# Optimization experiments

Hardware: AMD Instinct MI355X
Metric: run time of the kernel (lower is better)

The kernel has to match this reference:

```python
import jax, jax.numpy as jnp
import numpy as np

# pywt db4 decomposition lowpass filter (L=8)
DB4_DEC_LO = np.array([
    -0.010597401784997278, 0.032883011666982945, 0.030841381835986965,
    -0.18703481171888114, -0.02798376941698385, 0.6308807679295904,
    0.7148465705525415, 0.23037781330885523], dtype=np.float32)


def _dwt_1d(x, dec_lo, axis):
    """Single-level 1-D DWT along `axis`, pywt 'symmetric' mode.

    Implements pywt downsampling convolution: symmetric-extend by L-1 on each
    side, correlate with reversed decomposition filters, take every 2nd sample
    starting at offset 1. out_len = floor((n + L - 1) / 2).
    """
    L = dec_lo.shape[0]
    # QMF highpass: dec_hi[n] = (-1)^(n+1) * dec_lo[L-1-n]
    signs = jnp.where(jnp.arange(L) % 2 == 0, -1.0, 1.0).astype(x.dtype)
    dec_hi = signs * dec_lo[::-1]
    lo_rev = dec_lo[::-1]  # correlation kernel = reversed conv filter
    hi_rev = dec_hi[::-1]

    x = jnp.moveaxis(x, axis, -1)
    n = x.shape[-1]
    pad = [(0, 0)] * (x.ndim - 1) + [(L - 1, L - 1)]
    xp = jnp.pad(x, pad, mode='symmetric')  # half-sample symmetric, as pywt
    out_len = (n + L - 1) // 2

    ylo = jnp.zeros(x.shape[:-1] + (out_len,), x.dtype)
    yhi = jnp.zeros(x.shape[:-1] + (out_len,), x.dtype)
    for m in range(L):  # small fixed tap count; fused by XLA
        seg = xp[..., 1 + m: 1 + m + 2 * out_len: 2]
        ylo = ylo + lo_rev[m] * seg
        yhi = yhi + hi_rev[m] * seg
    return jnp.moveaxis(ylo, -1, axis), jnp.moveaxis(yhi, -1, axis)


def setup_inputs() -> dict:
    key = jax.random.key(0)
    x = jax.random.normal(key, (8, 512, 512, 16), dtype=jnp.float32)
    dec_lo = jnp.asarray(DB4_DEC_LO)
    return {"x": x, "dec_lo": dec_lo}


def reference(x, dec_lo):
    # Separable 2-D DWT over axes [-3, -2] (channels-last [B,H,W,C]).
    a, d = _dwt_1d(x, dec_lo, axis=-3)          # lowpass/highpass along H
    aa, ad = _dwt_1d(a, dec_lo, axis=-2)        # then along W
    da, dd = _dwt_1d(d, dec_lo, axis=-2)
    return (aa, ad, da, dd)
```

## Files before the change

kernel.cpp:

```cpp
#include <hip/hip_runtime.h>


constexpr int N  = 512;
constexpr int ON = 259;
constexpr int CH = 16;
constexpr int NB = 8;
constexpr int JB = 29;
constexpr int BANDS = 9;
constexpr int RS = 16;
constexpr int SEGS = 17;
constexpr int W  = 2 * JB + 6;
constexpr int LSTR = 20;

typedef float vfloat4 __attribute__((ext_vector_type(4)));

__device__ __forceinline__ int refl(int r) {
  r = (r < 0) ? (-r - 1) : r;
  return (r >= N) ? (2 * N - 1 - r) : r;
}

__device__ __forceinline__ int lds_idx(int c, int w) {
  return c * LSTR + ((w + ((c >> 2) << 2)) & 15);
}

__device__ __forceinline__ void block_sync_lds() {
  asm volatile("s_waitcnt lgkmcnt(0)" ::: "memory");
  __builtin_amdgcn_s_barrier();
  __builtin_amdgcn_sched_barrier(0);
}

__device__ __forceinline__ void nt_store4(float* p, float4 v) {
  vfloat4 nv = {v.x, v.y, v.z, v.w};
  __builtin_nontemporal_store(nv, reinterpret_cast<vfloat4*>(p));
}

__global__ __launch_bounds__(256) void dwt2_ring(
    const float* __restrict__ x, const float* __restrict__ dec_lo,
    float* __restrict__ out)
{
  const int band = blockIdx.x, seg = blockIdx.y, b = blockIdx.z;
  const int j0 = band * JB;
  const int i0 = seg * RS;
  const int t  = threadIdx.x;
  const int tc = t >> 2;
  const int tch = (t & 3) << 2;

  __shared__ float a_buf[2][W * LSTR];
  __shared__ float d_buf[2][W * LSTR];

  float lo[8], hi[8];
#pragma unroll
  for (int m = 0; m < 8; ++m) lo[m] = dec_lo[7 - m];
#pragma unroll
  for (int m = 0; m < 8; ++m) hi[m] = (m & 1) ? -dec_lo[m] : dec_lo[m];

  const int gc = refl(2 * j0 - 6 + tc);
  const float* xb   = x + (size_t)b * N * N * CH;
  const float* colp = xb + (size_t)gc * CH + tch;

  auto ldrow = [&](int r) -> float4 {
    return *reinterpret_cast<const float4*>(colp + (size_t)refl(r) * (N * CH));
  };

  float4 f[8];
#pragma unroll
  for (int m = 0; m < 8; ++m) f[m] = ldrow(2 * i0 - 6 + m);

  const int  sb  = (t >= 116);
  const int  p   = sb ? (t - 116) : t;
  const int  jr  = p >> 2;
  const int  bch = (p & 3) << 2;
  const int  j   = j0 + jr;
  const bool wr  = (t < 232) && (j < ON);
  const size_t OUTSZ = (size_t)NB * ON * ON * CH;
  float* o_lo = out + (size_t)(2 * sb) * OUTSZ;
  float* o_hi = o_lo + OUTSZ;

  const int widx = lds_idx(tc, tch);

#pragma unroll
  for (int it = 0; it < RS; ++it) {
    const int i = i0 + it;
    const int cur = it & 1;

    float4 av = {0.f, 0.f, 0.f, 0.f}, dv = {0.f, 0.f, 0.f, 0.f};
#pragma unroll
    for (int m = 0; m < 8; ++m) {
      av.x += lo[m] * f[m].x; av.y += lo[m] * f[m].y;
      av.z += lo[m] * f[m].z; av.w += lo[m] * f[m].w;
      dv.x += hi[m] * f[m].x; dv.y += hi[m] * f[m].y;
      dv.z += hi[m] * f[m].z; dv.w += hi[m] * f[m].w;
    }

#pragma unroll
    for (int k = 0; k < 6; ++k) f[k] = f[k + 2];
    if (it + 1 < RS) {
      f[6] = ldrow(2 * i + 2);
      f[7] = ldrow(2 * i + 3);
    }

    *reinterpret_cast<float4*>(&a_buf[cur][widx]) = av;
    *reinterpret_cast<float4*>(&d_buf[cur][widx]) = dv;

    block_sync_lds();

    if (wr && i < ON) {
      const float* src = sb ? d_buf[cur] : a_buf[cur];
      float4 aL = {0.f, 0.f, 0.f, 0.f}, aH = {0.f, 0.f, 0.f, 0.f};
#pragma unroll
      for (int m = 0; m < 8; ++m) {
        const float4 s = *reinterpret_cast<const float4*>(
            &src[lds_idx(2 * jr + m, bch)]);
        aL.x += lo[m] * s.x; aL.y += lo[m] * s.y;
        aL.z += lo[m] * s.z; aL.w += lo[m] * s.w;
        aH.x += hi[m] * s.x; aH.y += hi[m] * s.y;
        aH.z += hi[m] * s.z; aH.w += hi[m] * s.w;
      }
      const size_t o = (((size_t)b * ON + i) * ON + j) * CH + bch;
      nt_store4(o_lo + o, aL);
      nt_store4(o_hi + o, aH);
    }
  }
}

extern "C" void kernel_launch(void* const* d_in, const int* in_sizes, int n_in,
                              void* d_out, int out_size, void* d_ws, size_t ws_size,
                              hipStream_t stream) {
  const float* x      = (const float*)d_in[0];
  const float* dec_lo = (const float*)d_in[1];
  float* out          = (float*)d_out;
  dim3 grid(BANDS, SEGS, NB);
  dwt2_ring<<<grid, 256, 0, stream>>>(x, dec_lo, out);
}
```

Baseline: 56.12 us.

## Widen column bands so each thread handles two input columns and outputs

Column band width grows from 29 to 61 outputs, so there are 5 bands instead of 9. Each thread now loads and filters two input columns along H, and the W-pass work is split into up to two output slots per thread. Wider bands cut the redundant halo columns that neighbouring bands both load (6 extra columns per band), which lowers global read traffic. In exchange the grid has fewer blocks (680 instead of 1224), each thread uses more registers, and the W-pass load per thread is uneven.

```diff
diff --git a/kernel.cpp b/kernel.cpp
--- a/kernel.cpp
+++ b/kernel.cpp
@@ -5,8 +5,8 @@
 constexpr int ON = 259;
 constexpr int CH = 16;
 constexpr int NB = 8;
-constexpr int JB = 29;
-constexpr int BANDS = 9;
+constexpr int JB = 61;
+constexpr int BANDS = 5;
 constexpr int RS = 16;
 constexpr int SEGS = 17;
 constexpr int W  = 2 * JB + 6;
@@ -42,7 +42,7 @@
   const int j0 = band * JB;
   const int i0 = seg * RS;
   const int t  = threadIdx.x;
-  const int tc = t >> 2;
+  const int tc  = t >> 2;
   const int tch = (t & 3) << 2;
 
   __shared__ float a_buf[2][W * LSTR];
@@ -54,71 +54,117 @@
 #pragma unroll
   for (int m = 0; m < 8; ++m) hi[m] = (m & 1) ? -dec_lo[m] : dec_lo[m];
 
-  const int gc = refl(2 * j0 - 6 + tc);
-  const float* xb   = x + (size_t)b * N * N * CH;
-  const float* colp = xb + (size_t)gc * CH + tch;
+  const int c0 = tc, c1 = tc + 64;
+  const int gc0 = refl(2 * j0 - 6 + c0);
+  const int gc1 = refl(2 * j0 - 6 + c1);
+  const float* xb = x + (size_t)b * N * N * CH;
+  const float* colp0 = xb + (size_t)gc0 * CH + tch;
+  const float* colp1 = xb + (size_t)gc1 * CH + tch;
 
-  auto ldrow = [&](int r) -> float4 {
-    return *reinterpret_cast<const float4*>(colp + (size_t)refl(r) * (N * CH));
+  auto ldrow0 = [&](int r) -> float4 {
+    return *reinterpret_cast<const float4*>(colp0 + (size_t)refl(r) * (N * CH));
+  };
+  auto ldrow1 = [&](int r) -> float4 {
+    return *reinterpret_cast<const float4*>(colp1 + (size_t)refl(r) * (N * CH));
   };
 
-  float4 f[8];
+  float4 f0[8], f1[8];
 #pragma unroll
-  for (int m = 0; m < 8; ++m) f[m] = ldrow(2 * i0 - 6 + m);
+  for (int m = 0; m < 8; ++m) f0[m] = ldrow0(2 * i0 - 6 + m);
+#pragma unroll
+  for (int m = 0; m < 8; ++m) f1[m] = ldrow1(2 * i0 - 6 + m);
 
-  const int  sb  = (t >= 116);
-  const int  p   = sb ? (t - 116) : t;
-  const int  jr  = p >> 2;
-  const int  bch = (p & 3) << 2;
-  const int  j   = j0 + jr;
-  const bool wr  = (t < 232) && (j < ON);
   const size_t OUTSZ = (size_t)NB * ON * ON * CH;
-  float* o_lo = out + (size_t)(2 * sb) * OUTSZ;
-  float* o_hi = o_lo + OUTSZ;
 
-  const int widx = lds_idx(tc, tch);
+  const int q0 = t;
+  const int sb0 = (q0 >= 244);
+  const int p0  = q0 - 244 * sb0;
+  const int jr0 = p0 >> 2, bw0 = (p0 & 3) << 2;
+  const int jA  = j0 + jr0;
+  const bool v0ok = (jA < ON);
+  float* o_lo0 = out + (size_t)(2 * sb0) * OUTSZ;
+  float* o_hi0 = o_lo0 + OUTSZ;
+
+  const int q1 = t + 256;
+  const bool q1valid = (q1 < 488);
+  const int sb1 = 1;
+  const int p1  = q1 - 244;
+  const int jr1 = p1 >> 2, bw1 = (p1 & 3) << 2;
+  const int jB  = j0 + jr1;
+  const bool v1ok = q1valid && (jB < ON);
+  float* o_lo1 = out + (size_t)(2 * sb1) * OUTSZ;
+  float* o_hi1 = o_lo1 + OUTSZ;
+
+  const int widx0 = lds_idx(c0, tch);
+  const int widx1 = lds_idx(c1, tch);
 
 #pragma unroll
   for (int it = 0; it < RS; ++it) {
     const int i = i0 + it;
     const int cur = it & 1;
 
-    float4 av = {0.f, 0.f, 0.f, 0.f}, dv = {0.f, 0.f, 0.f, 0.f};
+    float4 av0 = {0,0,0,0}, dv0 = {0,0,0,0}, av1 = {0,0,0,0}, dv1 = {0,0,0,0};
 #pragma unroll
     for (int m = 0; m < 8; ++m) {
-      av.x += lo[m] * f[m].x; av.y += lo[m] * f[m].y;
-      av.z += lo[m] * f[m].z; av.w += lo[m] * f[m].w;
-      dv.x += hi[m] * f[m].x; dv.y += hi[m] * f[m].y;
-      dv.z += hi[m] * f[m].z; dv.w += hi[m] * f[m].w;
+      av0.x += lo[m] * f0[m].x; av0.y += lo[m] * f0[m].y;
+      av0.z += lo[m] * f0[m].z; av0.w += lo[m] * f0[m].w;
+      dv0.x += hi[m] * f0[m].x; dv0.y += hi[m] * f0[m].y;
+      dv0.z += hi[m] * f0[m].z; dv0.w += hi[m] * f0[m].w;
+      av1.x += lo[m] * f1[m].x; av1.y += lo[m] * f1[m].y;
+      av1.z += lo[m] * f1[m].z; av1.w += lo[m] * f1[m].w;
+      dv1.x += hi[m] * f1[m].x; dv1.y += hi[m] * f1[m].y;
+      dv1.z += hi[m] * f1[m].z; dv1.w += hi[m] * f1[m].w;
     }
 
 #pragma unroll
-    for (int k = 0; k < 6; ++k) f[k] = f[k + 2];
+    for (int k = 0; k < 6; ++k) { f0[k] = f0[k + 2]; f1[k] = f1[k + 2]; }
     if (it + 1 < RS) {
-      f[6] = ldrow(2 * i + 2);
-      f[7] = ldrow(2 * i + 3);
+      f0[6] = ldrow0(2 * i + 2);
+      f0[7] = ldrow0(2 * i + 3);
+      f1[6] = ldrow1(2 * i + 2);
+      f1[7] = ldrow1(2 * i + 3);
     }
 
-    *reinterpret_cast<float4*>(&a_buf[cur][widx]) = av;
-    *reinterpret_cast<float4*>(&d_buf[cur][widx]) = dv;
+    *reinterpret_cast<float4*>(&a_buf[cur][widx0]) = av0;
+    *reinterpret_cast<float4*>(&d_buf[cur][widx0]) = dv0;
+    *reinterpret_cast<float4*>(&a_buf[cur][widx1]) = av1;
+    *reinterpret_cast<float4*>(&d_buf[cur][widx1]) = dv1;
 
     block_sync_lds();
 
-    if (wr && i < ON) {
-      const float* src = sb ? d_buf[cur] : a_buf[cur];
-      float4 aL = {0.f, 0.f, 0.f, 0.f}, aH = {0.f, 0.f, 0.f, 0.f};
+    if (i < ON) {
+      if (v0ok) {
+        const float* src = sb0 ? d_buf[cur] : a_buf[cur];
+        float4 aL = {0,0,0,0}, aH = {0,0,0,0};
 #pragma unroll
-      for (int m = 0; m < 8; ++m) {
-        const float4 s = *reinterpret_cast<const float4*>(
-            &src[lds_idx(2 * jr + m, bch)]);
-        aL.x += lo[m] * s.x; aL.y += lo[m] * s.y;
-        aL.z += lo[m] * s.z; aL.w += lo[m] * s.w;
-        aH.x += hi[m] * s.x; aH.y += hi[m] * s.y;
-        aH.z += hi[m] * s.z; aH.w += hi[m] * s.w;
+        for (int m = 0; m < 8; ++m) {
+          const float4 s = *reinterpret_cast<const float4*>(
+              &src[lds_idx(2 * jr0 + m, bw0)]);
+          aL.x += lo[m] * s.x; aL.y += lo[m] * s.y;
+          aL.z += lo[m] * s.z; aL.w += lo[m] * s.w;
+          aH.x += hi[m] * s.x; aH.y += hi[m] * s.y;
+          aH.z += hi[m] * s.z; aH.w += hi[m] * s.w;
+        }
+        const size_t o = (((size_t)b * ON + i) * ON + jA) * CH + bw0;
+        nt_store4(o_lo0 + o, aL);
+        nt_store4(o_hi0 + o, aH);
       }
-      const size_t o = (((size_t)b * ON + i) * ON + j) * CH + bch;
-      nt_store4(o_lo + o, aL);
-      nt_store4(o_hi + o, aH);
+      if (v1ok) {
+        const float* src = d_buf[cur];
+        float4 aL = {0,0,0,0}, aH = {0,0,0,0};
+#pragma unroll
+        for (int m = 0; m < 8; ++m) {
+          const float4 s = *reinterpret_cast<const float4*>(
+              &src[lds_idx(2 * jr1 + m, bw1)]);
+          aL.x += lo[m] * s.x; aL.y += lo[m] * s.y;
+          aL.z += lo[m] * s.z; aL.w += lo[m] * s.w;
+          aH.x += hi[m] * s.x; aH.y += hi[m] * s.y;
+          aH.z += hi[m] * s.z; aH.w += hi[m] * s.w;
+        }
+        const size_t o = (((size_t)b * ON + i) * ON + jB) * CH + bw1;
+        nt_store4(o_lo1 + o, aL);
+        nt_store4(o_hi1 + o, aH);
+      }
     }
   }
 }
```

After: 58.35 us. 1.04x slower.
